# Kernel tuning notes

Measured on AMD Instinct MI355X. Metric: run time of the kernel, lower is better.

## Reference

```python
import jax, jax.numpy as jnp
import numpy as np

B, S, H = 1, 2048, 1024
NH, NKV, HD = 16, 4, 64  # n_attn_heads, n_kv_heads, head_dim


def setup_inputs() -> dict:
    key = jax.random.key(0)
    k1, k2, k3, k4 = jax.random.split(key, 4)
    x = jax.random.normal(k1, (B, S, H), dtype=jnp.float32)
    Wq = jax.random.normal(k2, (H, H), dtype=jnp.float32) * 0.02
    Wk = jax.random.normal(k3, (NKV * HD, H), dtype=jnp.float32) * 0.02
    Wv = jax.random.normal(k4, (NKV * HD, H), dtype=jnp.float32) * 0.02
    return {"x": x, "Wq": Wq, "Wk": Wk, "Wv": Wv}


def reference(x, Wq, Wk, Wv):
    b, s, h = x.shape
    rep = NH // NKV
    # projections (torch Linear: x @ W.T)
    q = (x @ Wq.T).reshape(b, s, NH, HD).transpose(0, 2, 1, 3)      # [b, NH, s, d]
    k = (x @ Wk.T).reshape(b, s, NKV, HD).transpose(0, 2, 1, 3)     # [b, NKV, s, d]
    v = (x @ Wv.T).reshape(b, s, NKV, HD).transpose(0, 2, 1, 3)
    # repeat_kv: expand each kv head rep times
    k = jnp.repeat(k, rep, axis=1)                                   # [b, NH, s, d]
    v = jnp.repeat(v, rep, axis=1)
    # NOTE: source scales by 1/sqrt(hidden_size), not 1/sqrt(head_dim)
    scale = 1.0 / np.sqrt(H).astype(np.float32)
    scores = jnp.einsum('bhqd,bhkd->bhqk', q, k) * scale             # [b, NH, s, s]
    causal = jnp.tril(jnp.ones((s, s), dtype=bool))
    scores = jnp.where(causal[None, None], scores, -jnp.inf)
    probs = jax.nn.softmax(scores, axis=-1)
    y = jnp.einsum('bhqk,bhkd->bhqd', probs, v)                      # [b, NH, s, d]
    return y.transpose(0, 2, 1, 3).reshape(b, s, NH * HD)
```

## Files before the change

kernel.cpp:

```cpp
#include <hip/hip_runtime.h>

#define S_LEN 2048
#define HID   1024
#define NHEAD 16
#define NKVH  4
#define HDIM  64
#define QKSTR 1280

typedef __bf16 bf16x8 __attribute__((ext_vector_type(8)));
typedef __bf16 bf16x4 __attribute__((ext_vector_type(4)));
typedef float  f32x4  __attribute__((ext_vector_type(4)));
typedef short  s16x4  __attribute__((ext_vector_type(4)));

#define QSCALE 0.04508422f

__device__ __forceinline__ unsigned short f2bf(float f) {
    unsigned u = __builtin_bit_cast(unsigned, f);
    u = u + 0x7FFFu + ((u >> 16) & 1u);
    return (unsigned short)(u >> 16);
}

__device__ __forceinline__ bf16x8 cvt8(float4 a, float4 b) {
    bf16x8 r;
    r[0] = (__bf16)a.x; r[1] = (__bf16)a.y; r[2] = (__bf16)a.z; r[3] = (__bf16)a.w;
    r[4] = (__bf16)b.x; r[5] = (__bf16)b.y; r[6] = (__bf16)b.z; r[7] = (__bf16)b.w;
    return r;
}

__device__ __forceinline__ f32x4 mfma_16x16x16_bf16(s16x4 a, s16x4 b, f32x4 c) {
#if __has_builtin(__builtin_amdgcn_mfma_f32_16x16x16bf16_1k)
    return __builtin_amdgcn_mfma_f32_16x16x16bf16_1k(a, b, c, 0, 0, 0);
#else
    f32x4 d = c;
    asm volatile("s_nop 1\n\tv_mfma_f32_16x16x16_bf16 %0, %1, %2, %0\n\ts_nop 3"
                 : "+v"(d) : "v"(a), "v"(b));
    return d;
#endif
}

__global__ __launch_bounds__(256, 2) void proj_gemm(
    const float* __restrict__ x,  const float* __restrict__ wq,
    const float* __restrict__ wk, const float* __restrict__ wv,
    unsigned short* __restrict__ qkv,
    unsigned short* __restrict__ vT)
{
    __shared__ unsigned short At[2][64 * 64];
    __shared__ unsigned short Bt[2][96 * 64];
    const int tid = threadIdx.x;
    const int w = tid >> 6, l = tid & 63;
    const int quad = l >> 4, lane16 = l & 15;
    const int m0 = blockIdx.y * 64, n0 = blockIdx.x * 96;
    const int wm = (w & 1) * 32, wn = (w >> 1) * 48;

    const int srow = l >> 3;
    const int scol = ((l & 7) ^ srow) * 8;
    const int dcol = (l & 7) * 8;

    f32x4 acc[2][3] = {};
    float4 arA[2][2], arB[3][2];

    #define PLOAD(KT)                                                                   \
        do {                                                                            \
            _Pragma("unroll")                                                           \
            for (int c = 0; c < 2; ++c) {                                               \
                const float* ga = x + (long)(m0 + w * 16 + c * 8 + srow) * HID          \
                                    + (KT) + scol;                                      \
                arA[c][0] = ((const float4*)ga)[0];                                     \
                arA[c][1] = ((const float4*)ga)[1];                                     \
            }                                                                           \
            _Pragma("unroll")                                                           \
            for (int c = 0; c < 3; ++c) {                                               \
                const int row = n0 + w * 24 + c * 8 + srow;                             \
                const float* gb = (row < 1024) ? wq + (long)row * HID                   \
                                : (row < 1280) ? wk + (long)(row - 1024) * HID          \
                                               : wv + (long)(row - 1280) * HID;         \
                gb += (KT) + scol;                                                      \
                arB[c][0] = ((const float4*)gb)[0];                                     \
                arB[c][1] = ((const float4*)gb)[1];                                     \
            }                                                                           \
        } while (0)

    #define PWRITE(BUF)                                                                 \
        do {                                                                            \
            _Pragma("unroll")                                                           \
            for (int c = 0; c < 2; ++c)                                                 \
                *(bf16x8*)&At[BUF][(w * 16 + c * 8 + srow) * 64 + dcol] =               \
                    cvt8(arA[c][0], arA[c][1]);                                         \
            _Pragma("unroll")                                                           \
            for (int c = 0; c < 3; ++c)                                                 \
                *(bf16x8*)&Bt[BUF][(w * 24 + c * 8 + srow) * 64 + dcol] =               \
                    cvt8(arB[c][0], arB[c][1]);                                         \
        } while (0)

    PLOAD(0);

    for (int i = 0; i < 16; ++i) {
        const int cur = i & 1;
        PWRITE(cur);
        __syncthreads();
        if (i + 1 < 16) PLOAD((i + 1) * 64);

        #pragma unroll
        for (int ks = 0; ks < 2; ++ks) {
            const int swz = ((ks * 4 + quad) ^ (lane16 & 7)) * 8;
            bf16x8 a[2], b[3];
            #pragma unroll
            for (int mi = 0; mi < 2; ++mi)
                a[mi] = *(const bf16x8*)&At[cur][(wm + mi * 16 + lane16) * 64 + swz];
            #pragma unroll
            for (int ni = 0; ni < 3; ++ni)
                b[ni] = *(const bf16x8*)&Bt[cur][(wn + ni * 16 + lane16) * 64 + swz];
            #pragma unroll
            for (int mi = 0; mi < 2; ++mi)
                #pragma unroll
                for (int ni = 0; ni < 3; ++ni)
                    acc[mi][ni] = __builtin_amdgcn_mfma_f32_16x16x32_bf16(a[mi], b[ni], acc[mi][ni], 0, 0, 0);
        }
    }
    #undef PLOAD
    #undef PWRITE

    #pragma unroll
    for (int mi = 0; mi < 2; ++mi) {
        const int row = m0 + wm + mi * 16 + quad * 4;
        #pragma unroll
        for (int ni = 0; ni < 3; ++ni) {
            const int col = n0 + wn + ni * 16 + lane16;
            #pragma unroll
            for (int r = 0; r < 4; ++r) {
                const float v = acc[mi][ni][r];
                if (col < 1024)
                    qkv[(long)(row + r) * QKSTR + col] = f2bf(v * QSCALE);
                else if (col < 1280)
                    qkv[(long)(row + r) * QKSTR + col] = f2bf(v);
                else
                    vT[(long)(col - 1280) * S_LEN + (row + r)] = f2bf(v);
            }
        }
    }
}

#define KSTR 72
__global__ __launch_bounds__(256, 4) void attn(
    const unsigned short* __restrict__ qkv,
    const unsigned short* __restrict__ vT,
    float* __restrict__ opart,
    float* __restrict__ rpart)
{
    __shared__ unsigned short Kt[2][64 * KSTR];
    __shared__ unsigned short Vt[2][64 * KSTR];

    const int tid = threadIdx.x;
    const int w = tid >> 6, l = tid & 63;
    const int quad = l >> 4, lane16 = l & 15;
    const int bx = blockIdx.x, by = blockIdx.y, bz = blockIdx.z;
    const int qt = (by & 8) ? (31 - bx) : bx;
    const int h  = by;
    const int kh = h >> 2;
    const int qcol = h * 64;
    const int kcol = 1024 + kh * 64;

    const int nt  = qt + 1;
    const int h1  = (nt + 1) >> 1;
    const int tlo = bz ? h1 : 0;
    const int thi = bz ? nt : h1;

    const long qrow = (long)(qt * 64 + w * 16 + lane16);
    bf16x8 qa0 = *(const bf16x8*)&qkv[qrow * QKSTR + qcol + quad * 8];
    bf16x8 qa1 = *(const bf16x8*)&qkv[qrow * QKSTR + qcol + 32 + quad * 8];

    f32x4 oT[4] = {};
    float rsum[4] = {0.f, 0.f, 0.f, 0.f};

    const int sr = tid >> 2, ss = tid & 3;
    const long vrow = (long)(kh * 64 + sr) * S_LEN;

    bf16x8 kr0, kr1, vr0, vr1;
    if (tlo < thi) {
        const long gk = (long)(tlo * 64 + sr) * QKSTR + kcol + ss * 16;
        kr0 = *(const bf16x8*)&qkv[gk];
        kr1 = *(const bf16x8*)&qkv[gk + 8];
        const long gv = vrow + tlo * 64 + ss * 16;
        vr0 = *(const bf16x8*)&vT[gv];
        vr1 = *(const bf16x8*)&vT[gv + 8];
    }

    for (int kt = tlo; kt < thi; ++kt) {
        const int cur = kt & 1;
        *(bf16x8*)&Kt[cur][sr * KSTR + ss * 16]     = kr0;
        *(bf16x8*)&Kt[cur][sr * KSTR + ss * 16 + 8] = kr1;
        *(bf16x8*)&Vt[cur][sr * KSTR + ss * 16]     = vr0;
        *(bf16x8*)&Vt[cur][sr * KSTR + ss * 16 + 8] = vr1;

        __syncthreads();

        if (kt + 1 < thi) {
            const long gk = (long)((kt + 1) * 64 + sr) * QKSTR + kcol + ss * 16;
            kr0 = *(const bf16x8*)&qkv[gk];
            kr1 = *(const bf16x8*)&qkv[gk + 8];
            const long gv = vrow + (kt + 1) * 64 + ss * 16;
            vr0 = *(const bf16x8*)&vT[gv];
            vr1 = *(const bf16x8*)&vT[gv + 8];
        }

        f32x4 sacc[4] = {};
        __builtin_amdgcn_s_setprio(1);
        #pragma unroll
        for (int t = 0; t < 4; ++t) {
            bf16x8 kb0 = *(const bf16x8*)&Kt[cur][(t * 16 + lane16) * KSTR + quad * 8];
            bf16x8 kb1 = *(const bf16x8*)&Kt[cur][(t * 16 + lane16) * KSTR + 32 + quad * 8];
            sacc[t] = __builtin_amdgcn_mfma_f32_16x16x32_bf16(kb0, qa0, sacc[t], 0, 0, 0);
            sacc[t] = __builtin_amdgcn_mfma_f32_16x16x32_bf16(kb1, qa1, sacc[t], 0, 0, 0);
        }
        __builtin_amdgcn_s_setprio(0);

        if (kt == qt) {
            #pragma unroll
            for (int t = 0; t < 4; ++t) {
                const int kvw = t * 16 + quad * 4;
                #pragma unroll
                for (int r = 0; r < 4; ++r)
                    if (kvw + r > w * 16 + lane16) sacc[t][r] = -3.0e38f;
            }
        }

        s16x4 pfrag[4];
        #pragma unroll
        for (int t = 0; t < 4; ++t) {
            const float p0 = __builtin_amdgcn_exp2f(sacc[t][0]);
            const float p1 = __builtin_amdgcn_exp2f(sacc[t][1]);
            const float p2 = __builtin_amdgcn_exp2f(sacc[t][2]);
            const float p3 = __builtin_amdgcn_exp2f(sacc[t][3]);
            rsum[t] += (p0 + p1) + (p2 + p3);
            bf16x4 pk;
            pk[0] = (__bf16)p0; pk[1] = (__bf16)p1;
            pk[2] = (__bf16)p2; pk[3] = (__bf16)p3;
            pfrag[t] = __builtin_bit_cast(s16x4, pk);
        }

        __builtin_amdgcn_s_setprio(1);
        #pragma unroll
        for (int dt = 0; dt < 4; ++dt)
            #pragma unroll
            for (int t = 0; t < 4; ++t) {
                bf16x4 va = *(const bf16x4*)&Vt[cur][(dt * 16 + lane16) * KSTR + t * 16 + quad * 4];
                oT[dt] = mfma_16x16x16_bf16(__builtin_bit_cast(s16x4, va), pfrag[t], oT[dt]);
            }
        __builtin_amdgcn_s_setprio(0);
    }

    float total = (rsum[0] + rsum[1]) + (rsum[2] + rsum[3]);
    total += __shfl_xor(total, 16);
    total += __shfl_xor(total, 32);

    float* op = opart + (long)bz * S_LEN * (NHEAD * HDIM);
    #pragma unroll
    for (int dt = 0; dt < 4; ++dt) {
        const int col = h * 64 + dt * 16 + quad * 4;
        float4 v; v.x = oT[dt][0]; v.y = oT[dt][1]; v.z = oT[dt][2]; v.w = oT[dt][3];
        *(float4*)&op[qrow * (NHEAD * HDIM) + col] = v;
    }
    if (l < 16)
        rpart[(long)bz * NHEAD * S_LEN + (long)h * S_LEN + qrow] = total;
}

__global__ __launch_bounds__(256) void combine(
    const float* __restrict__ opart, const float* __restrict__ rpart,
    float* __restrict__ out)
{
    const long idx = (long)blockIdx.x * 256 + threadIdx.x;
    const long row = idx >> 8;
    const int  c4  = (int)(idx & 255);
    const int  col = c4 * 4;
    const int  h   = col >> 6;

    const float4 a = *(const float4*)&opart[row * 1024 + col];
    const float4 b = *(const float4*)&opart[(long)S_LEN * 1024 + row * 1024 + col];
    const float r  = rpart[(long)h * S_LEN + row] +
                     rpart[(long)NHEAD * S_LEN + (long)h * S_LEN + row];
    const float inv = 1.0f / r;
    float4 o;
    o.x = (a.x + b.x) * inv; o.y = (a.y + b.y) * inv;
    o.z = (a.z + b.z) * inv; o.w = (a.w + b.w) * inv;
    *(float4*)&out[row * 1024 + col] = o;
}

extern "C" void kernel_launch(void* const* d_in, const int* in_sizes, int n_in,
                              void* d_out, int out_size, void* d_ws, size_t ws_size,
                              hipStream_t stream) {
    const float* x  = (const float*)d_in[0];
    const float* wq = (const float*)d_in[1];
    const float* wk = (const float*)d_in[2];
    const float* wv = (const float*)d_in[3];
    float* out = (float*)d_out;

    unsigned short* qkv = (unsigned short*)d_ws;
    unsigned short* vT  = qkv + (size_t)S_LEN * QKSTR;
    float* opart = (float*)(vT + (size_t)256 * S_LEN);
    float* rpart = opart + (size_t)2 * S_LEN * (NHEAD * HDIM);

    proj_gemm<<<dim3(16, 32), dim3(256), 0, stream>>>(x, wq, wk, wv, qkv, vT);
    attn<<<dim3(32, 16, 2), dim3(256), 0, stream>>>(qkv, vT, opart, rpart);
    combine<<<dim3(2048), dim3(256), 0, stream>>>(opart, rpart, out);
}
```

Before: 114.4 us.

## Fuse split-K combine into attention via atomic ticket per tile

Removes the separate combine kernel. Each attention block writes its partial output, then takes an atomic ticket on a per-tile flag, and the second finisher merges the other half's partial with its own registers and writes the normalized output. Flags are zeroed by the projection kernel. This saves a launch and one full read of both partials, at the cost of fences, an atomic per block, and reliance on memory visibility across blocks.

Result: slower. 297.8 us (+160.4%).

```diff
diff --git a/kernel.cpp b/kernel.cpp
--- a/kernel.cpp
+++ b/kernel.cpp
@@ -42,7 +42,8 @@
     const float* __restrict__ x,  const float* __restrict__ wq,
     const float* __restrict__ wk, const float* __restrict__ wv,
     unsigned short* __restrict__ qkv,
-    unsigned short* __restrict__ vT)
+    unsigned short* __restrict__ vT,
+    unsigned int* __restrict__ flags)
 {
     __shared__ unsigned short At[2][64 * 64];
     __shared__ unsigned short Bt[2][96 * 64];
@@ -51,6 +52,11 @@
     const int quad = l >> 4, lane16 = l & 15;
     const int m0 = blockIdx.y * 64, n0 = blockIdx.x * 96;
     const int wm = (w & 1) * 32, wn = (w >> 1) * 48;
+
+    if (blockIdx.x == 0 && blockIdx.y == 0) {
+        flags[tid] = 0u;
+        flags[256 + tid] = 0u;
+    }
 
     const int srow = l >> 3;
     const int scol = ((l & 7) ^ srow) * 8;
@@ -145,10 +151,13 @@
     const unsigned short* __restrict__ qkv,
     const unsigned short* __restrict__ vT,
     float* __restrict__ opart,
-    float* __restrict__ rpart)
+    float* __restrict__ rpart,
+    unsigned int* __restrict__ flags,
+    float* __restrict__ out)
 {
     __shared__ unsigned short Kt[2][64 * KSTR];
     __shared__ unsigned short Vt[2][64 * KSTR];
+    __shared__ int ticket_s;
 
     const int tid = threadIdx.x;
     const int w = tid >> 6, l = tid & 63;
@@ -262,27 +271,28 @@
     }
     if (l < 16)
         rpart[(long)bz * NHEAD * S_LEN + (long)h * S_LEN + qrow] = total;
-}
-
-__global__ __launch_bounds__(256) void combine(
-    const float* __restrict__ opart, const float* __restrict__ rpart,
-    float* __restrict__ out)
-{
-    const long idx = (long)blockIdx.x * 256 + threadIdx.x;
-    const long row = idx >> 8;
-    const int  c4  = (int)(idx & 255);
-    const int  col = c4 * 4;
-    const int  h   = col >> 6;
-
-    const float4 a = *(const float4*)&opart[row * 1024 + col];
-    const float4 b = *(const float4*)&opart[(long)S_LEN * 1024 + row * 1024 + col];
-    const float r  = rpart[(long)h * S_LEN + row] +
-                     rpart[(long)NHEAD * S_LEN + (long)h * S_LEN + row];
-    const float inv = 1.0f / r;
-    float4 o;
-    o.x = (a.x + b.x) * inv; o.y = (a.y + b.y) * inv;
-    o.z = (a.z + b.z) * inv; o.w = (a.w + b.w) * inv;
-    *(float4*)&out[row * 1024 + col] = o;
+
+    __threadfence();
+    if (tid == 0)
+        ticket_s = (int)atomicAdd(&flags[by * 32 + bx], 1u);
+    __syncthreads();
+    if (ticket_s == 1) {
+        __threadfence();
+        const float* pop = opart + (long)(bz ^ 1) * S_LEN * (NHEAD * HDIM);
+        const float r2 = rpart[(long)(bz ^ 1) * NHEAD * S_LEN + (long)h * S_LEN + qrow];
+        const float inv = 1.0f / (total + r2);
+        #pragma unroll
+        for (int dt = 0; dt < 4; ++dt) {
+            const int col = h * 64 + dt * 16 + quad * 4;
+            const float4 pv = *(const float4*)&pop[qrow * (NHEAD * HDIM) + col];
+            float4 o;
+            o.x = (oT[dt][0] + pv.x) * inv;
+            o.y = (oT[dt][1] + pv.y) * inv;
+            o.z = (oT[dt][2] + pv.z) * inv;
+            o.w = (oT[dt][3] + pv.w) * inv;
+            *(float4*)&out[qrow * (NHEAD * HDIM) + col] = o;
+        }
+    }
 }
 
 extern "C" void kernel_launch(void* const* d_in, const int* in_sizes, int n_in,
@@ -298,8 +308,8 @@
     unsigned short* vT  = qkv + (size_t)S_LEN * QKSTR;
     float* opart = (float*)(vT + (size_t)256 * S_LEN);
     float* rpart = opart + (size_t)2 * S_LEN * (NHEAD * HDIM);
-
-    proj_gemm<<<dim3(16, 32), dim3(256), 0, stream>>>(x, wq, wk, wv, qkv, vT);
-    attn<<<dim3(32, 16, 2), dim3(256), 0, stream>>>(qkv, vT, opart, rpart);
-    combine<<<dim3(2048), dim3(256), 0, stream>>>(opart, rpart, out);
-}
+    unsigned int* flags = (unsigned int*)(rpart + (size_t)2 * NHEAD * S_LEN);
+
+    proj_gemm<<<dim3(16, 32), dim3(256), 0, stream>>>(x, wq, wk, wv, qkv, vT, flags);
+    attn<<<dim3(32, 16, 2), dim3(256), 0, stream>>>(qkv, vT, opart, rpart, flags, out);
+}
```
